# Kernel tuning notes

Measured on AMD Instinct MI355X. Metric: run time of the kernel, lower is better.

Reference implementation:

```python
import jax, jax.numpy as jnp
import numpy as np

SEQ_LEN = 512
MAX_SPAN = 15
BATCH = 8
HIDDEN = 1024
WIDTH_DIM = 64
NUM_LABELS = 3


def _enumerate_spans(seq_len, max_span):
    starts, ends = [], []
    for s in range(seq_len):
        for e in range(s, min(s + max_span, seq_len)):
            starts.append(s)
            ends.append(e)
    return np.asarray(starts, np.int32), np.asarray(ends, np.int32)


def setup_inputs() -> dict:
    key = jax.random.key(0)
    k = jax.random.split(key, 6)
    starts, ends = _enumerate_spans(SEQ_LEN, MAX_SPAN)  # N = 7575
    d_in = HIDDEN * 2 + WIDTH_DIM  # 2112
    return {
        "sequence_output": jax.random.normal(k[0], (BATCH, SEQ_LEN, HIDDEN), jnp.float32),
        "width_emb": jax.random.normal(k[1], (MAX_SPAN, WIDTH_DIM), jnp.float32) * 0.02,
        "W1": jax.random.normal(k[2], (d_in, HIDDEN), jnp.float32) * (1.0 / np.sqrt(d_in)),
        "b1": jnp.zeros((HIDDEN,), jnp.float32),
        "W2": jax.random.normal(k[3], (HIDDEN, NUM_LABELS), jnp.float32) * (1.0 / np.sqrt(HIDDEN)),
        "b2": jnp.zeros((NUM_LABELS,), jnp.float32),
        "span_starts": jnp.asarray(starts),
        "span_ends": jnp.asarray(ends),
    }


def reference(sequence_output, width_emb, W1, b1, W2, b2, span_starts, span_ends):
    # Gather start/end token representations for every candidate span.
    B = sequence_output.shape[0]
    N = span_starts.shape[0]
    start_repr = sequence_output[:, span_starts]            # [B, N, H]
    end_repr = sequence_output[:, span_ends]                # [B, N, H]
    width_repr = width_emb[span_ends - span_starts]         # [N, 64]
    width_repr = jnp.broadcast_to(width_repr[None], (B, N, width_repr.shape[-1]))
    span_reprs = jnp.concatenate([start_repr, end_repr, width_repr], axis=-1)  # [B, N, 2H+64]
    # Span classifier MLP (dropout is identity in eval mode).
    h = jax.nn.relu(jnp.einsum("bnd,dh->bnh", span_reprs, W1) + b1)
    logits = jnp.einsum("bnh,hl->bnl", h, W2) + b2          # [B, N, num_labels]
    return logits
```

## Files before the change

### kernel.cpp

```cpp
#include <hip/hip_runtime.h>
#include <stdint.h>

#define SEQ 512
#define BATCH 8
#define HID 1024

typedef __attribute__((ext_vector_type(8))) __bf16 bf16x8;
typedef __attribute__((ext_vector_type(4))) float f32x4;
typedef __attribute__((ext_vector_type(2))) float f32x2;

__device__ __forceinline__ unsigned short f2bf(float f) {
    unsigned int u = __float_as_uint(f);
    unsigned int r = 0x7fffu + ((u >> 16) & 1u);
    return (unsigned short)((u + r) >> 16);
}

__device__ __forceinline__ void unpack8(uint4 v, float* f) {
    f[0] = __uint_as_float(v.x << 16);
    f[1] = __uint_as_float(v.x & 0xffff0000u);
    f[2] = __uint_as_float(v.y << 16);
    f[3] = __uint_as_float(v.y & 0xffff0000u);
    f[4] = __uint_as_float(v.z << 16);
    f[5] = __uint_as_float(v.z & 0xffff0000u);
    f[6] = __uint_as_float(v.w << 16);
    f[7] = __uint_as_float(v.w & 0xffff0000u);
}

__device__ __forceinline__ f32x2 up2(unsigned int v) {
    f32x2 r;
    r.x = __uint_as_float(v << 16);
    r.y = __uint_as_float(v & 0xffff0000u);
    return r;
}

template <int CTRL>
__device__ __forceinline__ float dpp_add(float x) {
    int t = __builtin_amdgcn_update_dpp(0, __float_as_int(x), CTRL, 0xf, 0xf, true);
    return x + __int_as_float(t);
}
__device__ __forceinline__ float wave_sum63(float x) {
    x = dpp_add<0x111>(x);
    x = dpp_add<0x112>(x);
    x = dpp_add<0x114>(x);
    x = dpp_add<0x118>(x);
    x = dpp_add<0x142>(x);
    x = dpp_add<0x143>(x);
    return x;
}

__global__ __launch_bounds__(256) void k_prep(const float* __restrict__ seq,
                                              const float* __restrict__ wemb,
                                              const float* __restrict__ W1,
                                              const float* __restrict__ b1,
                                              const float* __restrict__ W2,
                                              ushort* __restrict__ seqb,
                                              ushort* __restrict__ Bt,
                                              float* __restrict__ Rf,
                                              float* __restrict__ W2t) {
    __shared__ float tile[32][33];
    const int bid = blockIdx.x;
    const int tid = threadIdx.x;
    if (bid < 60) {
        int idx = bid * 256 + tid;
        int w = idx >> 10, j = idx & 1023;
        float a0 = b1[j], a1 = 0.f, a2 = 0.f, a3 = 0.f;
#pragma unroll
        for (int c = 0; c < 64; c += 4) {
            a0 = fmaf(wemb[w * 64 + c + 0], W1[(size_t)(2048 + c + 0) * 1024 + j], a0);
            a1 = fmaf(wemb[w * 64 + c + 1], W1[(size_t)(2048 + c + 1) * 1024 + j], a1);
            a2 = fmaf(wemb[w * 64 + c + 2], W1[(size_t)(2048 + c + 2) * 1024 + j], a2);
            a3 = fmaf(wemb[w * 64 + c + 3], W1[(size_t)(2048 + c + 3) * 1024 + j], a3);
        }
        Rf[idx] = (a0 + a1) + (a2 + a3);
    } else if (bid < 72) {
        int idx = (bid - 60) * 256 + tid;
        int l = idx >> 10, j = idx & 1023;
        W2t[idx] = W2[j * 3 + l];
    } else if (bid < 4168) {
        int i = (bid - 72) * 256 + tid;
        float4 v = ((const float4*)seq)[i];
        ushort4 o;
        o.x = f2bf(v.x); o.y = f2bf(v.y); o.z = f2bf(v.z); o.w = f2bf(v.w);
        ((ushort4*)seqb)[i] = o;
    } else {
        int idx = bid - 4168;
        int nb = (idx & 63) * 32, kb = (idx >> 6) * 32;
        int tx = tid & 31, ty = tid >> 5;
        int n = nb + tx;
        int rb = (n < 1024) ? 0 : 1024;
        int nc = n - rb;
#pragma unroll
        for (int i = 0; i < 4; ++i) {
            int k = kb + ty + i * 8;
            tile[ty + i * 8][tx] = W1[(size_t)(rb + k) * 1024 + nc];
        }
        __syncthreads();
#pragma unroll
        for (int i = 0; i < 4; ++i) {
            int n2 = nb + ty + i * 8;
            Bt[(size_t)n2 * 1024 + kb + tx] = f2bf(tile[tx][ty + i * 8]);
        }
    }
}

__global__ __launch_bounds__(256) void k_gemm(const ushort* __restrict__ A,
                                              const ushort* __restrict__ Bt,
                                              ushort* __restrict__ P,
                                              ushort* __restrict__ Q) {
    __shared__ ushort Al[2][8192];
    __shared__ ushort Bl[2][8192];
    const int tid = threadIdx.x;
    const int wid = tid >> 6;
    const int lane = tid & 63;
    const int bid = blockIdx.x;
    const int x = bid & 7, t8 = bid >> 3;
    const int m0 = (((x >> 1) << 3) + (t8 >> 3)) * 128;
    const int n0 = (((x & 1) << 3) + (t8 & 7)) * 128;
    const int wm = (wid >> 1) * 64;
    const int wn = (wid & 1) * 64;
    const int srow = lane >> 2;
    const int scol = (lane & 3) * 8;
    const int fr = lane & 15;
    const int fk = (lane >> 4) * 8;

    f32x4 acc[4][4] = {};

    const ushort* Abase = A  + (size_t)(m0 + srow) * 1024 + scol;
    const ushort* Bbase = Bt + (size_t)(n0 + srow) * 1024 + scol;

#define STAGE(buf, k0)                                                                     \
    {                                                                                      \
        _Pragma("unroll")                                                                  \
        for (int r = 0; r < 4; ++r) {                                                      \
            int c = wid + 4 * r;                                                           \
            int half = c >> 3;                                                             \
            int rows = (c & 7) * 16;                                                       \
            const ushort* sa = Abase + (size_t)rows * 1024 + (k0) + half * 32;             \
            const ushort* sb = Bbase + (size_t)rows * 1024 + (k0) + half * 32;             \
            int loff = half * 4096 + rows * 32;                                            \
            __builtin_amdgcn_global_load_lds((const __attribute__((address_space(1))) void*)sa, \
                                             (__attribute__((address_space(3))) void*)(&Al[buf][loff]), \
                                             16, 0, 0);                                    \
            __builtin_amdgcn_global_load_lds((const __attribute__((address_space(1))) void*)sb, \
                                             (__attribute__((address_space(3))) void*)(&Bl[buf][loff]), \
                                             16, 0, 0);                                    \
        }                                                                                  \
    }

#define COMPUTE(cur)                                                                       \
    {                                                                                      \
        _Pragma("unroll")                                                                  \
        for (int kk = 0; kk < 2; ++kk) {                                                   \
            bf16x8 af[4], bg[4];                                                           \
            _Pragma("unroll")                                                              \
            for (int i = 0; i < 4; ++i)                                                    \
                af[i] = *(const bf16x8*)(&Al[cur][kk * 4096 + (wm + i * 16 + fr) * 32 + fk]); \
            _Pragma("unroll")                                                              \
            for (int j = 0; j < 4; ++j)                                                    \
                bg[j] = *(const bf16x8*)(&Bl[cur][kk * 4096 + (wn + j * 16 + fr) * 32 + fk]); \
            __builtin_amdgcn_s_setprio(1);                                                 \
            _Pragma("unroll")                                                              \
            for (int i = 0; i < 4; ++i)                                                    \
                _Pragma("unroll")                                                          \
                for (int j = 0; j < 4; ++j)                                                \
                    acc[i][j] = __builtin_amdgcn_mfma_f32_16x16x32_bf16(af[i], bg[j], acc[i][j], 0, 0, 0); \
            __builtin_amdgcn_s_setprio(0);                                                 \
        }                                                                                  \
    }

    STAGE(0, 0);
    for (int t = 0; t < 15; ++t) {
        const int cur = t & 1;
        STAGE(cur ^ 1, (t + 1) * 64);
        asm volatile("s_waitcnt vmcnt(8)" ::: "memory");
        __builtin_amdgcn_s_barrier();
        COMPUTE(cur);
        __builtin_amdgcn_s_barrier();
    }
    asm volatile("s_waitcnt vmcnt(0)" ::: "memory");
    __builtin_amdgcn_s_barrier();
    COMPUTE(1);
#undef STAGE
#undef COMPUTE

    ushort* Cb = (n0 < 1024) ? P : Q;
    const int nc0 = n0 & 1023;
    const int cr = (lane >> 4) * 4;
    const int cc = lane & 15;
#pragma unroll
    for (int i = 0; i < 4; ++i)
#pragma unroll
        for (int j = 0; j < 4; ++j) {
            ushort* Cp = Cb + (size_t)(m0 + wm + i * 16 + cr) * 1024 + (nc0 + wn + j * 16 + cc);
#pragma unroll
            for (int r = 0; r < 4; ++r)
                Cp[(size_t)r * 1024] = f2bf(acc[i][j][r]);
        }
}

__global__ __launch_bounds__(512, 2) void k_span8(const ushort* __restrict__ Pmat,
                                                  const ushort* __restrict__ Qmat,
                                                  const float* __restrict__ Rf,
                                                  const float* __restrict__ W2t,
                                                  const float* __restrict__ b2,
                                                  float* __restrict__ out, int nspans) {
    __shared__ float Rs[15 * 1024];
    const int tid = threadIdx.x;
    const int wid = tid >> 6, lane = tid & 63;
    const int b = blockIdx.x >> 6;
    const int s0 = (blockIdx.x & 63) << 3;

#pragma unroll
    for (int i = 0; i < 8; ++i) {
        int c = wid + (i << 3);
        if (c < 60) {
            int g = (c << 8) + lane * 4;
            __builtin_amdgcn_global_load_lds((const __attribute__((address_space(1))) void*)(Rf + g),
                                             (__attribute__((address_space(3))) void*)(Rs + g),
                                             16, 0, 0);
        }
    }

    f32x2 w2r2[3][2][4];
#pragma unroll
    for (int l = 0; l < 3; ++l)
#pragma unroll
        for (int it = 0; it < 2; ++it) {
            const float4* p = (const float4*)(W2t + l * 1024 + it * 512 + lane * 8);
            float4 v0 = p[0], v1 = p[1];
            w2r2[l][it][0] = (f32x2){v0.x, v0.y};
            w2r2[l][it][1] = (f32x2){v0.z, v0.w};
            w2r2[l][it][2] = (f32x2){v1.x, v1.y};
            w2r2[l][it][3] = (f32x2){v1.z, v1.w};
        }
    const float bb0 = b2[0], bb1 = b2[1], bb2 = b2[2];

    const int s = s0 + wid;
    f32x2 pf2[8];
    {
        const uint4* pr = (const uint4*)(Pmat + (((size_t)(b << 9) + s) << 10) + lane * 8);
        uint4 p0 = pr[0], p1 = pr[64];
        pf2[0] = up2(p0.x); pf2[1] = up2(p0.y); pf2[2] = up2(p0.z); pf2[3] = up2(p0.w);
        pf2[4] = up2(p1.x); pf2[5] = up2(p1.y); pf2[6] = up2(p1.z); pf2[7] = up2(p1.w);
    }

    __syncthreads();

    const int rrem = SEQ - s;
    const int nsp = (rrem < 15) ? rrem : 15;
    const int off = (rrem >= 15) ? 15 * s : (7575 - (rrem * (rrem + 1)) / 2);
    float* op = out + ((size_t)b * nspans + off) * 3;

    const uint4* qp = (const uint4*)(Qmat + (((size_t)(b << 9) + s) << 10) + lane * 8);
    uint4 q0 = qp[0], q1 = qp[64];

    for (int w = 0; w < nsp; ++w) {
        uint4 nq0, nq1;
        if (w + 1 < nsp) {
            qp += 128;
            nq0 = qp[0]; nq1 = qp[64];
        } else {
            nq0 = q0; nq1 = q1;
        }
        f32x2 A0 = {0.f, 0.f}, A1 = {0.f, 0.f}, A2 = {0.f, 0.f};
#pragma unroll
        for (int it = 0; it < 2; ++it) {
            uint4 qv = (it == 0) ? q0 : q1;
            const float4* rp = (const float4*)(Rs + w * 1024 + it * 512 + lane * 8);
            float4 ra = rp[0], rb = rp[1];
            f32x2 q2[4] = {up2(qv.x), up2(qv.y), up2(qv.z), up2(qv.w)};
            f32x2 r2[4] = {(f32x2){ra.x, ra.y}, (f32x2){ra.z, ra.w},
                           (f32x2){rb.x, rb.y}, (f32x2){rb.z, rb.w}};
#pragma unroll
            for (int k = 0; k < 4; ++k) {
                f32x2 h = pf2[it * 4 + k] + q2[k] + r2[k];
                h.x = fmaxf(h.x, 0.f);
                h.y = fmaxf(h.y, 0.f);
                A0 += h * w2r2[0][it][k];
                A1 += h * w2r2[1][it][k];
                A2 += h * w2r2[2][it][k];
            }
        }
        float a0 = A0.x + A0.y;
        float a1 = A1.x + A1.y;
        float a2 = A2.x + A2.y;
        a0 = wave_sum63(a0);
        a1 = wave_sum63(a1);
        a2 = wave_sum63(a2);
        if (lane == 63) {
            op[w * 3 + 0] = a0 + bb0;
            op[w * 3 + 1] = a1 + bb1;
            op[w * 3 + 2] = a2 + bb2;
        }
        q0 = nq0; q1 = nq1;
    }
}

extern "C" void kernel_launch(void* const* d_in, const int* in_sizes, int n_in,
                              void* d_out, int out_size, void* d_ws, size_t ws_size,
                              hipStream_t stream) {
    const float* seq    = (const float*)d_in[0];
    const float* wemb   = (const float*)d_in[1];
    const float* W1     = (const float*)d_in[2];
    const float* b1     = (const float*)d_in[3];
    const float* W2     = (const float*)d_in[4];
    const float* b2     = (const float*)d_in[5];
    float* out = (float*)d_out;
    int nspans = in_sizes[6];

    char* ws = (char*)d_ws;
    ushort* seqb = (ushort*)ws;
    ushort* Bt   = (ushort*)(ws + (8u << 20));
    ushort* Pmat = (ushort*)(ws + (12u << 20));
    ushort* Qmat = (ushort*)(ws + (20u << 20));
    float*  Rf   = (float*)(ws + (28u << 20));
    float*  W2t  = (float*)(ws + (29u << 20));

    hipLaunchKernelGGL(k_prep, dim3(6216), dim3(256), 0, stream,
                       seq, wemb, W1, b1, W2, seqb, Bt, Rf, W2t);
    hipLaunchKernelGGL(k_gemm, dim3(512), dim3(256), 0, stream, seqb, Bt, Pmat, Qmat);
    hipLaunchKernelGGL(k_span8, dim3(BATCH * 64), dim3(512), 0, stream,
                       Pmat, Qmat, Rf, W2t, b2, out, nspans);
}
```

Before: 53.64 us.

## Move width/W2 prep into GEMM launch and unroll span loop by two

The width-embedding projection (Rf) and W2 transpose move out of the prep kernel into 72 extra blocks appended to the GEMM grid. Those blocks can run alongside the GEMM tiles instead of lengthening the bandwidth-bound prep pass. The span kernel now processes two widths per iteration: it issues four Q loads together and interleaves two independent accumulation chains and reductions, raising ILP in place of the old one-ahead software prefetch. This costs more registers under the 512-thread, 2-waves launch bound, and the extra GEMM blocks may cause tail imbalance.

```diff
diff --git a/kernel.cpp b/kernel.cpp
--- a/kernel.cpp
+++ b/kernel.cpp
@@ -13,17 +13,6 @@
     unsigned int u = __float_as_uint(f);
     unsigned int r = 0x7fffu + ((u >> 16) & 1u);
     return (unsigned short)((u + r) >> 16);
-}
-
-__device__ __forceinline__ void unpack8(uint4 v, float* f) {
-    f[0] = __uint_as_float(v.x << 16);
-    f[1] = __uint_as_float(v.x & 0xffff0000u);
-    f[2] = __uint_as_float(v.y << 16);
-    f[3] = __uint_as_float(v.y & 0xffff0000u);
-    f[4] = __uint_as_float(v.z << 16);
-    f[5] = __uint_as_float(v.z & 0xffff0000u);
-    f[6] = __uint_as_float(v.w << 16);
-    f[7] = __uint_as_float(v.w & 0xffff0000u);
 }
 
 __device__ __forceinline__ f32x2 up2(unsigned int v) {
@@ -49,41 +38,20 @@
 }
 
 __global__ __launch_bounds__(256) void k_prep(const float* __restrict__ seq,
-                                              const float* __restrict__ wemb,
                                               const float* __restrict__ W1,
-                                              const float* __restrict__ b1,
-                                              const float* __restrict__ W2,
                                               ushort* __restrict__ seqb,
-                                              ushort* __restrict__ Bt,
-                                              float* __restrict__ Rf,
-                                              float* __restrict__ W2t) {
+                                              ushort* __restrict__ Bt) {
     __shared__ float tile[32][33];
     const int bid = blockIdx.x;
     const int tid = threadIdx.x;
-    if (bid < 60) {
-        int idx = bid * 256 + tid;
-        int w = idx >> 10, j = idx & 1023;
-        float a0 = b1[j], a1 = 0.f, a2 = 0.f, a3 = 0.f;
-#pragma unroll
-        for (int c = 0; c < 64; c += 4) {
-            a0 = fmaf(wemb[w * 64 + c + 0], W1[(size_t)(2048 + c + 0) * 1024 + j], a0);
-            a1 = fmaf(wemb[w * 64 + c + 1], W1[(size_t)(2048 + c + 1) * 1024 + j], a1);
-            a2 = fmaf(wemb[w * 64 + c + 2], W1[(size_t)(2048 + c + 2) * 1024 + j], a2);
-            a3 = fmaf(wemb[w * 64 + c + 3], W1[(size_t)(2048 + c + 3) * 1024 + j], a3);
-        }
-        Rf[idx] = (a0 + a1) + (a2 + a3);
-    } else if (bid < 72) {
-        int idx = (bid - 60) * 256 + tid;
-        int l = idx >> 10, j = idx & 1023;
-        W2t[idx] = W2[j * 3 + l];
-    } else if (bid < 4168) {
-        int i = (bid - 72) * 256 + tid;
+    if (bid < 4096) {
+        int i = bid * 256 + tid;
         float4 v = ((const float4*)seq)[i];
         ushort4 o;
         o.x = f2bf(v.x); o.y = f2bf(v.y); o.z = f2bf(v.z); o.w = f2bf(v.w);
         ((ushort4*)seqb)[i] = o;
     } else {
-        int idx = bid - 4168;
+        int idx = bid - 4096;
         int nb = (idx & 63) * 32, kb = (idx >> 6) * 32;
         int tx = tid & 31, ty = tid >> 5;
         int n = nb + tx;
@@ -105,14 +73,40 @@
 
 __global__ __launch_bounds__(256) void k_gemm(const ushort* __restrict__ A,
                                               const ushort* __restrict__ Bt,
+                                              const float* __restrict__ wemb,
+                                              const float* __restrict__ W1,
+                                              const float* __restrict__ b1,
+                                              const float* __restrict__ W2,
                                               ushort* __restrict__ P,
-                                              ushort* __restrict__ Q) {
+                                              ushort* __restrict__ Q,
+                                              float* __restrict__ Rf,
+                                              float* __restrict__ W2t) {
     __shared__ ushort Al[2][8192];
     __shared__ ushort Bl[2][8192];
     const int tid = threadIdx.x;
+    const int bid = blockIdx.x;
+    if (bid >= 512) {
+        if (bid < 572) {
+            int idx = (bid - 512) * 256 + tid;
+            int w = idx >> 10, j = idx & 1023;
+            float a0 = b1[j], a1 = 0.f, a2 = 0.f, a3 = 0.f;
+#pragma unroll
+            for (int c = 0; c < 64; c += 4) {
+                a0 = fmaf(wemb[w * 64 + c + 0], W1[(size_t)(2048 + c + 0) * 1024 + j], a0);
+                a1 = fmaf(wemb[w * 64 + c + 1], W1[(size_t)(2048 + c + 1) * 1024 + j], a1);
+                a2 = fmaf(wemb[w * 64 + c + 2], W1[(size_t)(2048 + c + 2) * 1024 + j], a2);
+                a3 = fmaf(wemb[w * 64 + c + 3], W1[(size_t)(2048 + c + 3) * 1024 + j], a3);
+            }
+            Rf[idx] = (a0 + a1) + (a2 + a3);
+        } else {
+            int idx = (bid - 572) * 256 + tid;
+            int l = idx >> 10, j = idx & 1023;
+            W2t[idx] = W2[j * 3 + l];
+        }
+        return;
+    }
     const int wid = tid >> 6;
     const int lane = tid & 63;
-    const int bid = blockIdx.x;
     const int x = bid & 7, t8 = bid >> 3;
     const int m0 = (((x >> 1) << 3) + (t8 >> 3)) * 128;
     const int n0 = (((x & 1) << 3) + (t8 & 7)) * 128;
@@ -198,7 +192,7 @@
         }
 }
 
-__global__ __launch_bounds__(512, 2) void k_span8(const ushort* __restrict__ Pmat,
+__global__ __launch_bounds__(512, 2) void k_span9(const ushort* __restrict__ Pmat,
                                                   const ushort* __restrict__ Qmat,
                                                   const float* __restrict__ Rf,
                                                   const float* __restrict__ W2t,
@@ -252,20 +246,63 @@
     float* op = out + ((size_t)b * nspans + off) * 3;
 
     const uint4* qp = (const uint4*)(Qmat + (((size_t)(b << 9) + s) << 10) + lane * 8);
-    uint4 q0 = qp[0], q1 = qp[64];
-
-    for (int w = 0; w < nsp; ++w) {
-        uint4 nq0, nq1;
-        if (w + 1 < nsp) {
-            qp += 128;
-            nq0 = qp[0]; nq1 = qp[64];
-        } else {
-            nq0 = q0; nq1 = q1;
-        }
+
+    int w = 0;
+    for (; w + 1 < nsp; w += 2) {
+        uint4 qa0 = qp[0],   qa1 = qp[64];
+        uint4 qb0 = qp[128], qb1 = qp[192];
+        qp += 256;
         f32x2 A0 = {0.f, 0.f}, A1 = {0.f, 0.f}, A2 = {0.f, 0.f};
+        f32x2 B0 = {0.f, 0.f}, B1 = {0.f, 0.f}, B2 = {0.f, 0.f};
 #pragma unroll
         for (int it = 0; it < 2; ++it) {
-            uint4 qv = (it == 0) ? q0 : q1;
+            uint4 qvA = it ? qa1 : qa0;
+            uint4 qvB = it ? qb1 : qb0;
+            const float4* rpA = (const float4*)(Rs + w * 1024 + it * 512 + lane * 8);
+            const float4* rpB = (const float4*)(Rs + (w + 1) * 1024 + it * 512 + lane * 8);
+            float4 raA = rpA[0], rbA = rpA[1];
+            float4 raB = rpB[0], rbB = rpB[1];
+            f32x2 q2A[4] = {up2(qvA.x), up2(qvA.y), up2(qvA.z), up2(qvA.w)};
+            f32x2 q2B[4] = {up2(qvB.x), up2(qvB.y), up2(qvB.z), up2(qvB.w)};
+            f32x2 r2A[4] = {(f32x2){raA.x, raA.y}, (f32x2){raA.z, raA.w},
+                            (f32x2){rbA.x, rbA.y}, (f32x2){rbA.z, rbA.w}};
+            f32x2 r2B[4] = {(f32x2){raB.x, raB.y}, (f32x2){raB.z, raB.w},
+                            (f32x2){rbB.x, rbB.y}, (f32x2){rbB.z, rbB.w}};
+#pragma unroll
+            for (int k = 0; k < 4; ++k) {
+                f32x2 hA = pf2[it * 4 + k] + q2A[k] + r2A[k];
+                f32x2 hB = pf2[it * 4 + k] + q2B[k] + r2B[k];
+                hA.x = fmaxf(hA.x, 0.f); hA.y = fmaxf(hA.y, 0.f);
+                hB.x = fmaxf(hB.x, 0.f); hB.y = fmaxf(hB.y, 0.f);
+                A0 += hA * w2r2[0][it][k];
+                B0 += hB * w2r2[0][it][k];
+                A1 += hA * w2r2[1][it][k];
+                B1 += hB * w2r2[1][it][k];
+                A2 += hA * w2r2[2][it][k];
+                B2 += hB * w2r2[2][it][k];
+            }
+        }
+        float a0 = A0.x + A0.y, b0 = B0.x + B0.y;
+        float a1 = A1.x + A1.y, b1v = B1.x + B1.y;
+        float a2 = A2.x + A2.y, b2v = B2.x + B2.y;
+        a0 = wave_sum63(a0); b0 = wave_sum63(b0);
+        a1 = wave_sum63(a1); b1v = wave_sum63(b1v);
+        a2 = wave_sum63(a2); b2v = wave_sum63(b2v);
+        if (lane == 63) {
+            op[w * 3 + 0] = a0 + bb0;
+            op[w * 3 + 1] = a1 + bb1;
+            op[w * 3 + 2] = a2 + bb2;
+            op[w * 3 + 3] = b0 + bb0;
+            op[w * 3 + 4] = b1v + bb1;
+            op[w * 3 + 5] = b2v + bb2;
+        }
+    }
+    if (w < nsp) {
+        uint4 qa0 = qp[0], qa1 = qp[64];
+        f32x2 A0 = {0.f, 0.f}, A1 = {0.f, 0.f}, A2 = {0.f, 0.f};
+#pragma unroll
+        for (int it = 0; it < 2; ++it) {
+            uint4 qv = it ? qa1 : qa0;
             const float4* rp = (const float4*)(Rs + w * 1024 + it * 512 + lane * 8);
             float4 ra = rp[0], rb = rp[1];
             f32x2 q2[4] = {up2(qv.x), up2(qv.y), up2(qv.z), up2(qv.w)};
@@ -274,8 +311,7 @@
 #pragma unroll
             for (int k = 0; k < 4; ++k) {
                 f32x2 h = pf2[it * 4 + k] + q2[k] + r2[k];
-                h.x = fmaxf(h.x, 0.f);
-                h.y = fmaxf(h.y, 0.f);
+                h.x = fmaxf(h.x, 0.f); h.y = fmaxf(h.y, 0.f);
                 A0 += h * w2r2[0][it][k];
                 A1 += h * w2r2[1][it][k];
                 A2 += h * w2r2[2][it][k];
@@ -292,7 +328,6 @@
             op[w * 3 + 1] = a1 + bb1;
             op[w * 3 + 2] = a2 + bb2;
         }
-        q0 = nq0; q1 = nq1;
     }
 }
 
@@ -316,9 +351,9 @@
     float*  Rf   = (float*)(ws + (28u << 20));
     float*  W2t  = (float*)(ws + (29u << 20));
 
-    hipLaunchKernelGGL(k_prep, dim3(6216), dim3(256), 0, stream,
-                       seq, wemb, W1, b1, W2, seqb, Bt, Rf, W2t);
-    hipLaunchKernelGGL(k_gemm, dim3(512), dim3(256), 0, stream, seqb, Bt, Pmat, Qmat);
-    hipLaunchKernelGGL(k_span8, dim3(BATCH * 64), dim3(512), 0, stream,
+    hipLaunchKernelGGL(k_prep, dim3(6144), dim3(256), 0, stream, seq, W1, seqb, Bt);
+    hipLaunchKernelGGL(k_gemm, dim3(584), dim3(256), 0, stream,
+                       seqb, Bt, wemb, W1, b1, W2, Pmat, Qmat, Rf, W2t);
+    hipLaunchKernelGGL(k_span9, dim3(BATCH * 64), dim3(512), 0, stream,
                        Pmat, Qmat, Rf, W2t, b2, out, nspans);
 }
```

After: 53.17 us, median of 2. No clear change (-0.9%).
